# Kernel tuning notes

Measured on AMD Instinct MI355X. Metric: run time of the kernel, lower is better.

The kernel has to match this reference:

```python
import jax, jax.numpy as jnp
import numpy as np

B, T, C = 128, 256, 384
H, HD = 8, 48          # num_heads, head_dim
WINDOW = 64

def setup_inputs() -> dict:
    key = jax.random.key(0)
    ks = jax.random.split(key, 5)
    return {
        "x": jax.random.normal(ks[0], (B, T, C), dtype=jnp.float32),
        "W_qkv": jax.random.normal(ks[1], (C, 3 * C), dtype=jnp.float32) * (1.0 / np.sqrt(C)),
        "b_qkv": jax.random.normal(ks[2], (3 * C,), dtype=jnp.float32) * 0.02,
        "W_proj": jax.random.normal(ks[3], (C, C), dtype=jnp.float32) * (1.0 / np.sqrt(C)),
        "b_proj": jax.random.normal(ks[4], (C,), dtype=jnp.float32) * 0.02,
        "gate": jnp.ones((C,), dtype=jnp.float32),
    }

def reference(x, W_qkv, b_qkv, W_proj, b_proj, gate):
    Bx, Tx, Cx = x.shape
    qkv = x @ W_qkv + b_qkv                                   # [B,T,3C]
    q, k, v = jnp.split(qkv, 3, axis=-1)
    q = q.reshape(Bx, Tx, H, HD).transpose(0, 2, 1, 3)        # [B,H,T,hd]
    k = k.reshape(Bx, Tx, H, HD).transpose(0, 2, 1, 3)
    v = v.reshape(Bx, Tx, H, HD).transpose(0, 2, 1, 3)
    scale = 1.0 / np.sqrt(HD).astype(np.float32)
    att = jnp.einsum("bhqd,bhkd->bhqk", q, k) * scale        # [B,H,T,T]
    idx = jnp.arange(Tx)
    causal = idx[:, None] >= idx[None, :]                     # lower-tri
    local = jnp.abs(idx[None, :] - idx[:, None]) <= WINDOW
    mask = (causal & local)[None, None, :, :]
    att = jnp.where(mask, att, -jnp.inf)
    att = jax.nn.softmax(att, axis=-1)
    out = jnp.einsum("bhqk,bhkd->bhqd", att, v)               # [B,H,T,hd]
    out = out.transpose(0, 2, 1, 3).reshape(Bx, Tx, Cx)       # [B,T,C]
    return (out * gate) @ W_proj + b_proj
```

## Files before the change

### kernel.cpp

```cpp
#include <hip/hip_runtime.h>
#include <hip/hip_bf16.h>

typedef __attribute__((ext_vector_type(8))) short bf16x8;
typedef __attribute__((ext_vector_type(4))) float floatx4;

#define NB 128
#define NT 256
#define NC 384
#define NH 8
#define ND 48

static __device__ __forceinline__ unsigned short f2bf(float f) {
  __hip_bfloat16 h = __float2bfloat16(f);
  return __builtin_bit_cast(unsigned short, h);
}

static __device__ __forceinline__ void gload16(const unsigned short* g, unsigned short* l) {
  __builtin_amdgcn_global_load_lds(
      (const __attribute__((address_space(1))) void*)g,
      (__attribute__((address_space(3))) void*)l, 16, 0, 0);
}

__global__ __launch_bounds__(256) void k_prep(const float* __restrict__ x,
                                              const float* __restrict__ Wq,
                                              const float* __restrict__ Wp,
                                              const float* __restrict__ gate,
                                              unsigned short* __restrict__ xbf,
                                              unsigned short* __restrict__ WqT,
                                              unsigned short* __restrict__ WpT) {
  const int blk = blockIdx.x;
  const int t = threadIdx.x;
  if (blk < 144) {
    __shared__ float T[64][65];
    const float* src;
    unsigned short* dst;
    int N, kt, nt;
    const bool isWp = (blk >= 108);
    if (!isWp) { src = Wq; dst = WqT; N = 1152; kt = blk / 18; nt = blk % 18; }
    else { int b2 = blk - 108; src = Wp; dst = WpT; N = 384; kt = b2 / 6; nt = b2 % 6; }
    const int k0 = kt * 64, n0 = nt * 64;
    const int r = t >> 2, c = (t & 3) * 16;
    const float* s = src + (size_t)(k0 + r) * N + n0 + c;
#pragma unroll
    for (int i = 0; i < 4; ++i) *(float4*)&T[r][c + i * 4] = ((const float4*)s)[i];
    __syncthreads();
    float gv[16];
    if (isWp) {
#pragma unroll
      for (int i = 0; i < 4; ++i) *(float4*)&gv[i * 4] = ((const float4*)(gate + k0 + c))[i];
    } else {
#pragma unroll
      for (int i = 0; i < 16; ++i) gv[i] = 1.f;
    }
    unsigned short o[16];
#pragma unroll
    for (int i = 0; i < 16; ++i) o[i] = f2bf(T[c + i][r] * gv[i]);
    unsigned short* dp = dst + (size_t)(n0 + r) * 384 + k0 + c;
    *(bf16x8*)dp = *(bf16x8*)&o[0];
    *(bf16x8*)(dp + 8) = *(bf16x8*)&o[8];
  } else {
    const int n8 = (NB * NT * NC) / 8;
    int idx = (blk - 144) * 256 + t;
    const int stride = (gridDim.x - 144) * 256;
    for (; idx < n8; idx += stride) {
      const float* s = x + (size_t)idx * 8;
      float v[8];
      *(float4*)&v[0] = ((const float4*)s)[0];
      *(float4*)&v[4] = ((const float4*)s)[1];
      bf16x8 p;
#pragma unroll
      for (int i = 0; i < 8; ++i) p[i] = f2bf(v[i]);
      *(bf16x8*)(xbf + (size_t)idx * 8) = p;
    }
  }
}

#define STAGE_G(Ag, Bg, As, Bs, k0, buf)                                             \
  {                                                                                  \
    const int r0_ = (lane >> 2), sw0_ = 8 * ((lane & 3) ^ ((r0_ >> 1) & 3));         \
    const int r1_ = r0_ + 16,    sw1_ = 8 * ((lane & 3) ^ ((r1_ >> 1) & 3));         \
    gload16(Ag + (size_t)r0_ * 384 + (k0) + sw0_, As + (buf)*4096 + (w * 32) * 32);  \
    gload16(Ag + (size_t)r1_ * 384 + (k0) + sw1_, As + (buf)*4096 + (w * 32 + 16) * 32); \
    gload16(Bg + (size_t)r0_ * 384 + (k0) + sw0_, Bs + (buf)*4096 + (w * 32) * 32);  \
    gload16(Bg + (size_t)r1_ * 384 + (k0) + sw1_, Bs + (buf)*4096 + (w * 32 + 16) * 32); \
  }

#define GEMM_PIPE(Ag, Bg, As, Bs)                                                    \
  STAGE_G(Ag, Bg, As, Bs, 0, 0);                                                     \
  STAGE_G(Ag, Bg, As, Bs, 32, 1);                                                    \
  _Pragma("unroll") for (int t_ = 0; t_ < 12; ++t_) {                                \
    if (t_ < 11) asm volatile("s_waitcnt vmcnt(4)" ::: "memory");                    \
    else         asm volatile("s_waitcnt vmcnt(0)" ::: "memory");                    \
    __builtin_amdgcn_s_barrier();                                                    \
    if (t_ < 10) STAGE_G(Ag, Bg, As, Bs, (t_ + 2) * 32, (t_ + 2) % 3);               \
    const unsigned short* Ac_ = As + (t_ % 3) * 4096;                                \
    const unsigned short* Bc_ = Bs + (t_ % 3) * 4096;                                \
    bf16x8 a_[4], b_[4];                                                             \
    _Pragma("unroll") for (int mt = 0; mt < 4; ++mt) {                               \
      const int R = wm * 64 + mt * 16 + lq;                                          \
      a_[mt] = *(const bf16x8*)&Ac_[R * 32 + 8 * (lg ^ ((R >> 1) & 3))];             \
    }                                                                                \
    _Pragma("unroll") for (int nt = 0; nt < 4; ++nt) {                               \
      const int R = wn * 64 + nt * 16 + lq;                                          \
      b_[nt] = *(const bf16x8*)&Bc_[R * 32 + 8 * (lg ^ ((R >> 1) & 3))];             \
    }                                                                                \
    _Pragma("unroll") for (int mt = 0; mt < 4; ++mt)                                 \
      _Pragma("unroll") for (int nt = 0; nt < 4; ++nt)                               \
        acc[mt][nt] = __builtin_amdgcn_mfma_f32_16x16x32_bf16(a_[mt], b_[nt], acc[mt][nt], 0, 0, 0); \
  }

__global__ __launch_bounds__(256) void k_qkv(const unsigned short* __restrict__ xb,
                                             const unsigned short* __restrict__ WqT,
                                             const float* __restrict__ bq,
                                             unsigned short* __restrict__ qkv) {
  __shared__ __align__(16) unsigned short As[3 * 128 * 32];
  __shared__ __align__(16) unsigned short Bs[3 * 128 * 32];
  const int t = threadIdx.x, lane = t & 63, w = t >> 6;
  const int wm = w >> 1, wn = w & 1;
  const int lq = lane & 15, lg = lane >> 4;
  const int swz = (blockIdx.x & 7) * 288 + (blockIdx.x >> 3);
  const int m0 = (swz / 9) * 128, n0 = (swz % 9) * 128;
  const unsigned short* Ag = xb + (size_t)(m0 + w * 32) * 384;
  const unsigned short* Bg = WqT + (size_t)(n0 + w * 32) * 384;
  floatx4 acc[4][4] = {};

  GEMM_PIPE(Ag, Bg, As, Bs);

#pragma unroll
  for (int nt = 0; nt < 4; ++nt) {
    const int col = n0 + wn * 64 + nt * 16 + lq;
    const float bias = bq[col];
#pragma unroll
    for (int mt = 0; mt < 4; ++mt)
#pragma unroll
      for (int j = 0; j < 4; ++j) {
        const int row = m0 + wm * 64 + mt * 16 + lg * 4 + j;
        qkv[(size_t)row * 1152 + col] = f2bf(acc[mt][nt][j] + bias);
      }
  }
}

__global__ __launch_bounds__(256) void k_proj(const unsigned short* __restrict__ A,
                                              const unsigned short* __restrict__ WpT,
                                              const float* __restrict__ bp,
                                              float* __restrict__ out) {
  __shared__ __align__(16) unsigned short As[3 * 128 * 32];
  __shared__ __align__(16) unsigned short Bs[3 * 128 * 32];
  const int t = threadIdx.x, lane = t & 63, w = t >> 6;
  const int wm = w >> 1, wn = w & 1;
  const int lq = lane & 15, lg = lane >> 4;
  const int swz = (blockIdx.x & 7) * 96 + (blockIdx.x >> 3);
  const int m0 = (swz / 3) * 128, n0 = (swz % 3) * 128;
  const unsigned short* Ag = A + (size_t)(m0 + w * 32) * 384;
  const unsigned short* Bg = WpT + (size_t)(n0 + w * 32) * 384;
  floatx4 acc[4][4] = {};

  GEMM_PIPE(Ag, Bg, As, Bs);

#pragma unroll
  for (int nt = 0; nt < 4; ++nt) {
    const int col = n0 + wn * 64 + nt * 16 + lq;
    const float bias = bp[col];
#pragma unroll
    for (int mt = 0; mt < 4; ++mt)
#pragma unroll
      for (int j = 0; j < 4; ++j) {
        const int row = m0 + wm * 64 + mt * 16 + lg * 4 + j;
        out[(size_t)row * 384 + col] = acc[mt][nt][j] + bias;
      }
  }
}

__global__ __launch_bounds__(256) void k_attn(const unsigned short* __restrict__ qkv,
                                              unsigned short* __restrict__ attg) {
  __shared__ __align__(16) unsigned short Ks[128 * 72];
  __shared__ __align__(16) unsigned short Vt[48 * 152];
  __shared__ __align__(16) unsigned short Ps[4 * 16 * 104];
  const int t = threadIdx.x;
  const int blk = blockIdx.x;
  const int tile = blk & 3;
  const int bh = blk >> 2;
  const int b = bh >> 3, h = bh & 7;
  const int base = tile * 64;
  const unsigned short* qbase = qkv + (size_t)(b * NT) * 1152 + h * 48;
  const unsigned short* kbase = qbase + 384;
  const unsigned short* vbase = qbase + 768;

  if (t < 48) {
    bf16x8 z = {};
    *(bf16x8*)&Vt[t * 152 + 128] = z;
    *(bf16x8*)&Vt[t * 152 + 136] = z;
  }
  if (t < 128) {
    const int r = t, ka = base - 64 + r;
    unsigned short* dst = &Ks[r * 72];
    if (ka >= 0) {
      const unsigned short* src = kbase + (size_t)ka * 1152;
#pragma unroll
      for (int i = 0; i < 6; ++i) *(bf16x8*)(dst + i * 8) = *(const bf16x8*)(src + i * 8);
      bf16x8 z = {};
      *(bf16x8*)(dst + 48) = z;
      *(bf16x8*)(dst + 56) = z;
    } else {
      bf16x8 z = {};
#pragma unroll
      for (int i = 0; i < 8; ++i) *(bf16x8*)(dst + i * 8) = z;
    }
  } else {
    const int r = t - 128, ka = base - 64 + r;
    if (ka >= 0) {
      const unsigned short* src = vbase + (size_t)ka * 1152;
      bf16x8 vv[6];
#pragma unroll
      for (int i = 0; i < 6; ++i) vv[i] = *(const bf16x8*)(src + i * 8);
#pragma unroll
      for (int i = 0; i < 6; ++i)
#pragma unroll
        for (int j = 0; j < 8; ++j)
          Vt[(i * 8 + j) * 152 + r] = (unsigned short)vv[i][j];
    } else {
#pragma unroll
      for (int d = 0; d < 48; ++d) Vt[d * 152 + r] = 0;
    }
  }
  __syncthreads();

  const int lane = t & 63, w = t >> 6;
  const int lq = lane & 15, lg = lane >> 4;
  const int qs = base + w * 16;

  const unsigned short* qrow = qbase + (size_t)(qs + lq) * 1152;
  bf16x8 aq0 = *(const bf16x8*)(qrow + lg * 8);
  bf16x8 aq1 = {};
  if (lg < 2) aq1 = *(const bf16x8*)(qrow + 32 + lg * 8);

  floatx4 s[5];
#pragma unroll
  for (int kt = 0; kt < 5; ++kt) {
    const unsigned short* kr = &Ks[(w * 16 + kt * 16 + lq) * 72];
    bf16x8 kb0 = *(const bf16x8*)(kr + lg * 8);
    bf16x8 kb1 = *(const bf16x8*)(kr + 32 + lg * 8);
    floatx4 z = {};
    z = __builtin_amdgcn_mfma_f32_16x16x32_bf16(aq0, kb0, z, 0, 0, 0);
    z = __builtin_amdgcn_mfma_f32_16x16x32_bf16(aq1, kb1, z, 0, 0, 0);
    s[kt] = z;
  }

  const float scale = 0.14433756729740643f;
  floatx4 pj[5];
#pragma unroll
  for (int j = 0; j < 4; ++j) {
    const int qa = qs + lg * 4 + j;
    float mx = -1e30f;
    float sv[5];
    bool ok[5];
#pragma unroll
    for (int kt = 0; kt < 5; ++kt) {
      const int ka = base - 64 + w * 16 + kt * 16 + lq;
      sv[kt] = s[kt][j] * scale;
      ok[kt] = (ka >= 0) && (ka <= qa) && (qa - ka <= 64);
      if (ok[kt]) mx = fmaxf(mx, sv[kt]);
    }
#pragma unroll
    for (int dd = 1; dd < 16; dd <<= 1) mx = fmaxf(mx, __shfl_xor(mx, dd));
    float sum = 0.f;
#pragma unroll
    for (int kt = 0; kt < 5; ++kt) {
      float p = ok[kt] ? __expf(sv[kt] - mx) : 0.f;
      pj[kt][j] = p;
      sum += p;
    }
#pragma unroll
    for (int dd = 1; dd < 16; dd <<= 1) sum += __shfl_xor(sum, dd);
    const float inv = 1.f / sum;
#pragma unroll
    for (int kt = 0; kt < 5; ++kt) pj[kt][j] *= inv;
  }

  unsigned short* pw = &Ps[w * 16 * 104];
#pragma unroll
  for (int kt = 0; kt < 5; ++kt)
#pragma unroll
    for (int j = 0; j < 4; ++j)
      pw[(lg * 4 + j) * 104 + kt * 16 + lq] = f2bf(pj[kt][j]);
#pragma unroll
  for (int j = 0; j < 4; ++j) pw[lq * 104 + 80 + lg * 4 + j] = 0;

  floatx4 o[3] = {};
#pragma unroll
  for (int c = 0; c < 3; ++c) {
    bf16x8 ap = *(const bf16x8*)&pw[lq * 104 + c * 32 + lg * 8];
#pragma unroll
    for (int nt = 0; nt < 3; ++nt) {
      bf16x8 av = *(const bf16x8*)&Vt[(nt * 16 + lq) * 152 + w * 16 + c * 32 + lg * 8];
      o[nt] = __builtin_amdgcn_mfma_f32_16x16x32_bf16(ap, av, o[nt], 0, 0, 0);
    }
  }
#pragma unroll
  for (int nt = 0; nt < 3; ++nt) {
    const int d = nt * 16 + lq;
    const int c = h * ND + d;
#pragma unroll
    for (int j = 0; j < 4; ++j) {
      const int tt = qs + lg * 4 + j;
      attg[((size_t)b * NT + tt) * NC + c] = f2bf(o[nt][j]);
    }
  }
}

extern "C" void kernel_launch(void* const* d_in, const int* in_sizes, int n_in,
                              void* d_out, int out_size, void* d_ws, size_t ws_size,
                              hipStream_t stream) {
  const float* x    = (const float*)d_in[0];
  const float* Wq   = (const float*)d_in[1];
  const float* bq   = (const float*)d_in[2];
  const float* Wp   = (const float*)d_in[3];
  const float* bp   = (const float*)d_in[4];
  const float* gate = (const float*)d_in[5];

  const size_t nx = (size_t)NB * NT * NC;
  unsigned short* attg = (unsigned short*)d_ws;
  unsigned short* xbf  = attg + nx;
  unsigned short* qkvp = xbf + nx;
  unsigned short* WqT  = qkvp + (size_t)NB * NT * 1152;
  unsigned short* WpT  = WqT + (size_t)384 * 1152;
  float* out = (float*)d_out;

  k_prep<<<dim3(1680), 256, 0, stream>>>(x, Wq, Wp, gate, xbf, WqT, WpT);
  k_qkv<<<dim3(2304), 256, 0, stream>>>(xbf, WqT, bq, qkvp);
  k_attn<<<dim3(4096), 256, 0, stream>>>(qkvp, attg);
  k_proj<<<dim3(768), 256, 0, stream>>>(attg, WpT, bp, out);
}
```

Measured before the change: 121.8 us.

## Restructure GEMMs with resident B tile and write QKV in head-major planes

Both GEMMs now load a full 48x384 weight slice into LDS once per block and give each wave its own 64-row A stream. This removes the block-wide barriers from the k-loop. The QKV GEMM stages its output through LDS and writes it as contiguous [comp][b,h][T][48] planes, so the attention kernel reads K, V and Q rows with unit stride instead of a 1152-element stride. The cost is smaller N tiles (48 wide) with less reuse of A per block, more blocks, and higher LDS use per block, which may lower occupancy.

```diff
diff --git a/kernel.cpp b/kernel.cpp
--- a/kernel.cpp
+++ b/kernel.cpp
@@ -9,6 +9,7 @@
 #define NC 384
 #define NH 8
 #define ND 48
+#define CPLANE (128 * 8 * 256 * 48)
 
 static __device__ __forceinline__ unsigned short f2bf(float f) {
   __hip_bfloat16 h = __float2bfloat16(f);
@@ -75,37 +76,48 @@
   }
 }
 
-#define STAGE_G(Ag, Bg, As, Bs, k0, buf)                                             \
-  {                                                                                  \
-    const int r0_ = (lane >> 2), sw0_ = 8 * ((lane & 3) ^ ((r0_ >> 1) & 3));         \
-    const int r1_ = r0_ + 16,    sw1_ = 8 * ((lane & 3) ^ ((r1_ >> 1) & 3));         \
-    gload16(Ag + (size_t)r0_ * 384 + (k0) + sw0_, As + (buf)*4096 + (w * 32) * 32);  \
-    gload16(Ag + (size_t)r1_ * 384 + (k0) + sw1_, As + (buf)*4096 + (w * 32 + 16) * 32); \
-    gload16(Bg + (size_t)r0_ * 384 + (k0) + sw0_, Bs + (buf)*4096 + (w * 32) * 32);  \
-    gload16(Bg + (size_t)r1_ * 384 + (k0) + sw1_, Bs + (buf)*4096 + (w * 32 + 16) * 32); \
-  }
-
-#define GEMM_PIPE(Ag, Bg, As, Bs)                                                    \
-  STAGE_G(Ag, Bg, As, Bs, 0, 0);                                                     \
-  STAGE_G(Ag, Bg, As, Bs, 32, 1);                                                    \
-  _Pragma("unroll") for (int t_ = 0; t_ < 12; ++t_) {                                \
-    if (t_ < 11) asm volatile("s_waitcnt vmcnt(4)" ::: "memory");                    \
-    else         asm volatile("s_waitcnt vmcnt(0)" ::: "memory");                    \
-    __builtin_amdgcn_s_barrier();                                                    \
-    if (t_ < 10) STAGE_G(Ag, Bg, As, Bs, (t_ + 2) * 32, (t_ + 2) % 3);               \
-    const unsigned short* Ac_ = As + (t_ % 3) * 4096;                                \
-    const unsigned short* Bc_ = Bs + (t_ % 3) * 4096;                                \
-    bf16x8 a_[4], b_[4];                                                             \
-    _Pragma("unroll") for (int mt = 0; mt < 4; ++mt) {                               \
-      const int R = wm * 64 + mt * 16 + lq;                                          \
-      a_[mt] = *(const bf16x8*)&Ac_[R * 32 + 8 * (lg ^ ((R >> 1) & 3))];             \
-    }                                                                                \
-    _Pragma("unroll") for (int nt = 0; nt < 4; ++nt) {                               \
-      const int R = wn * 64 + nt * 16 + lq;                                          \
-      b_[nt] = *(const bf16x8*)&Bc_[R * 32 + 8 * (lg ^ ((R >> 1) & 3))];             \
-    }                                                                                \
-    _Pragma("unroll") for (int mt = 0; mt < 4; ++mt)                                 \
-      _Pragma("unroll") for (int nt = 0; nt < 4; ++nt)                               \
+#define STAGE_A(k0, buf)                                                              \
+  {                                                                                   \
+    _Pragma("unroll") for (int g = 0; g < 4; ++g) {                                   \
+      const int r_ = (lane >> 2) + 16 * g;                                            \
+      gload16(Ag + (size_t)r_ * 384 + (k0) + 8 * ((lane & 3) ^ ((r_ >> 1) & 3)),      \
+              Asl + (buf)*2048 + g * 512);                                            \
+    }                                                                                 \
+  }
+
+#define STAGE_B(WT)                                                                   \
+  {                                                                                   \
+    _Pragma("unroll") for (int cc = 0; cc < 9; ++cc) {                                \
+      const int idx_ = cc * 256 + t;                                                  \
+      const int r_ = idx_ / 48, kc_ = idx_ - r_ * 48;                                 \
+      bf16x8 v_ = *(const bf16x8*)((WT) + (size_t)(n0 + r_) * 384 + kc_ * 8);         \
+      *(bf16x8*)&Bs[r_ * 384 + 8 * (kc_ ^ (r_ & 7))] = v_;                            \
+    }                                                                                 \
+  }
+
+#define GEMM_NOBAR()                                                                  \
+  STAGE_A(0, 0);                                                                      \
+  STAGE_A(32, 1);                                                                     \
+  __syncthreads();                                  \
+  _Pragma("unroll") for (int t_ = 0; t_ < 12; ++t_) {                                 \
+    if (t_ < 11) asm volatile("s_waitcnt vmcnt(4)" ::: "memory");                     \
+    else         asm volatile("s_waitcnt vmcnt(0)" ::: "memory");                     \
+    __builtin_amdgcn_sched_barrier(0);                                                \
+    const unsigned short* Ac_ = Asl + (t_ & 1) * 2048;                                \
+    bf16x8 a_[4], b_[3];                                                              \
+    _Pragma("unroll") for (int mt = 0; mt < 4; ++mt) {                                \
+      const int R = mt * 16 + lq;                                                     \
+      a_[mt] = *(const bf16x8*)&Ac_[R * 32 + 8 * (lg ^ ((R >> 1) & 3))];              \
+    }                                                                                 \
+    _Pragma("unroll") for (int nt = 0; nt < 3; ++nt) {                                \
+      const int R = nt * 16 + lq;                                                     \
+      b_[nt] = *(const bf16x8*)&Bs[R * 384 + 8 * ((t_ * 4 + lg) ^ (R & 7))];          \
+    }                                                                                 \
+    asm volatile("s_waitcnt lgkmcnt(0)" ::: "memory");                                \
+    __builtin_amdgcn_sched_barrier(0);                                                \
+    if (t_ < 10) STAGE_A((t_ + 2) * 32, t_ & 1);                                      \
+    _Pragma("unroll") for (int mt = 0; mt < 4; ++mt)                                  \
+      _Pragma("unroll") for (int nt = 0; nt < 3; ++nt)                                \
         acc[mt][nt] = __builtin_amdgcn_mfma_f32_16x16x32_bf16(a_[mt], b_[nt], acc[mt][nt], 0, 0, 0); \
   }
 
@@ -113,30 +125,39 @@
                                              const unsigned short* __restrict__ WqT,
                                              const float* __restrict__ bq,
                                              unsigned short* __restrict__ qkv) {
-  __shared__ __align__(16) unsigned short As[3 * 128 * 32];
-  __shared__ __align__(16) unsigned short Bs[3 * 128 * 32];
+  __shared__ __align__(16) unsigned short Bs[48 * 384];
+  __shared__ __align__(16) unsigned short As[4 * 4096];
   const int t = threadIdx.x, lane = t & 63, w = t >> 6;
-  const int wm = w >> 1, wn = w & 1;
   const int lq = lane & 15, lg = lane >> 4;
-  const int swz = (blockIdx.x & 7) * 288 + (blockIdx.x >> 3);
-  const int m0 = (swz / 9) * 128, n0 = (swz % 9) * 128;
-  const unsigned short* Ag = xb + (size_t)(m0 + w * 32) * 384;
-  const unsigned short* Bg = WqT + (size_t)(n0 + w * 32) * 384;
-  floatx4 acc[4][4] = {};
-
-  GEMM_PIPE(Ag, Bg, As, Bs);
-
-#pragma unroll
-  for (int nt = 0; nt < 4; ++nt) {
-    const int col = n0 + wn * 64 + nt * 16 + lq;
-    const float bias = bq[col];
+  const int swz = (blockIdx.x & 7) * 384 + (blockIdx.x >> 3);
+  const int mblk = swz / 24, nblk = swz % 24;
+  const int m0 = mblk * 256, n0 = nblk * 48;
+  const unsigned short* Ag = xb + (size_t)(m0 + w * 64) * 384;
+  unsigned short* Asl = As + w * 4096;
+
+  STAGE_B(WqT);
+  floatx4 acc[4][3] = {};
+  GEMM_NOBAR();
+
+  const int comp = nblk >> 3, h = nblk & 7;
+#pragma unroll
+  for (int nt = 0; nt < 3; ++nt) {
+    const float bias = bq[n0 + nt * 16 + lq];
 #pragma unroll
     for (int mt = 0; mt < 4; ++mt)
 #pragma unroll
       for (int j = 0; j < 4; ++j) {
-        const int row = m0 + wm * 64 + mt * 16 + lg * 4 + j;
-        qkv[(size_t)row * 1152 + col] = f2bf(acc[mt][nt][j] + bias);
+        const int r = mt * 16 + lg * 4 + j;
+        Asl[r * 48 + nt * 16 + lq] = f2bf(acc[mt][nt][j] + bias);
       }
+  }
+  asm volatile("s_waitcnt lgkmcnt(0)" ::: "memory");
+  __builtin_amdgcn_sched_barrier(0);
+  const size_t base = (size_t)comp * CPLANE + ((size_t)(mblk * 8 + h) * 256 + w * 64) * 48;
+#pragma unroll
+  for (int i = 0; i < 6; ++i) {
+    bf16x8 v = *(const bf16x8*)&Asl[i * 512 + lane * 8];
+    *(bf16x8*)(qkv + base + i * 512 + lane * 8) = v;
   }
 }
 
@@ -144,28 +165,29 @@
                                               const unsigned short* __restrict__ WpT,
                                               const float* __restrict__ bp,
                                               float* __restrict__ out) {
-  __shared__ __align__(16) unsigned short As[3 * 128 * 32];
-  __shared__ __align__(16) unsigned short Bs[3 * 128 * 32];
+  __shared__ __align__(16) unsigned short Bs[48 * 384];
+  __shared__ __align__(16) unsigned short As[4 * 4096];
   const int t = threadIdx.x, lane = t & 63, w = t >> 6;
-  const int wm = w >> 1, wn = w & 1;
   const int lq = lane & 15, lg = lane >> 4;
-  const int swz = (blockIdx.x & 7) * 96 + (blockIdx.x >> 3);
-  const int m0 = (swz / 3) * 128, n0 = (swz % 3) * 128;
-  const unsigned short* Ag = A + (size_t)(m0 + w * 32) * 384;
-  const unsigned short* Bg = WpT + (size_t)(n0 + w * 32) * 384;
-  floatx4 acc[4][4] = {};
-
-  GEMM_PIPE(Ag, Bg, As, Bs);
-
-#pragma unroll
-  for (int nt = 0; nt < 4; ++nt) {
-    const int col = n0 + wn * 64 + nt * 16 + lq;
+  const int swz = (blockIdx.x & 7) * 128 + (blockIdx.x >> 3);
+  const int mblk = swz / 8, nblk = swz % 8;
+  const int m0 = mblk * 256, n0 = nblk * 48;
+  const unsigned short* Ag = A + (size_t)(m0 + w * 64) * 384;
+  unsigned short* Asl = As + w * 4096;
+
+  STAGE_B(WpT);
+  floatx4 acc[4][3] = {};
+  GEMM_NOBAR();
+
+#pragma unroll
+  for (int nt = 0; nt < 3; ++nt) {
+    const int col = n0 + nt * 16 + lq;
     const float bias = bp[col];
 #pragma unroll
     for (int mt = 0; mt < 4; ++mt)
 #pragma unroll
       for (int j = 0; j < 4; ++j) {
-        const int row = m0 + wm * 64 + mt * 16 + lg * 4 + j;
+        const int row = m0 + w * 64 + mt * 16 + lg * 4 + j;
         out[(size_t)row * 384 + col] = acc[mt][nt][j] + bias;
       }
   }
@@ -182,9 +204,10 @@
   const int bh = blk >> 2;
   const int b = bh >> 3, h = bh & 7;
   const int base = tile * 64;
-  const unsigned short* qbase = qkv + (size_t)(b * NT) * 1152 + h * 48;
-  const unsigned short* kbase = qbase + 384;
-  const unsigned short* vbase = qbase + 768;
+  const size_t kvoff = (size_t)bh * NT * ND;
+  const unsigned short* qptr = qkv + kvoff;
+  const unsigned short* kptr = qkv + (size_t)CPLANE + kvoff;
+  const unsigned short* vptr = qkv + (size_t)2 * CPLANE + kvoff;
 
   if (t < 48) {
     bf16x8 z = {};
@@ -195,7 +218,7 @@
     const int r = t, ka = base - 64 + r;
     unsigned short* dst = &Ks[r * 72];
     if (ka >= 0) {
-      const unsigned short* src = kbase + (size_t)ka * 1152;
+      const unsigned short* src = kptr + (size_t)ka * ND;
 #pragma unroll
       for (int i = 0; i < 6; ++i) *(bf16x8*)(dst + i * 8) = *(const bf16x8*)(src + i * 8);
       bf16x8 z = {};
@@ -209,7 +232,7 @@
   } else {
     const int r = t - 128, ka = base - 64 + r;
     if (ka >= 0) {
-      const unsigned short* src = vbase + (size_t)ka * 1152;
+      const unsigned short* src = vptr + (size_t)ka * ND;
       bf16x8 vv[6];
 #pragma unroll
       for (int i = 0; i < 6; ++i) vv[i] = *(const bf16x8*)(src + i * 8);
@@ -229,7 +252,7 @@
   const int lq = lane & 15, lg = lane >> 4;
   const int qs = base + w * 16;
 
-  const unsigned short* qrow = qbase + (size_t)(qs + lq) * 1152;
+  const unsigned short* qrow = qptr + (size_t)(qs + lq) * ND;
   bf16x8 aq0 = *(const bf16x8*)(qrow + lg * 8);
   bf16x8 aq1 = {};
   if (lg < 2) aq1 = *(const bf16x8*)(qrow + 32 + lg * 8);
@@ -322,12 +345,12 @@
   unsigned short* attg = (unsigned short*)d_ws;
   unsigned short* xbf  = attg + nx;
   unsigned short* qkvp = xbf + nx;
-  unsigned short* WqT  = qkvp + (size_t)NB * NT * 1152;
+  unsigned short* WqT  = qkvp + (size_t)3 * CPLANE;
   unsigned short* WpT  = WqT + (size_t)384 * 1152;
   float* out = (float*)d_out;
 
   k_prep<<<dim3(1680), 256, 0, stream>>>(x, Wq, Wp, gate, xbf, WqT, WpT);
-  k_qkv<<<dim3(2304), 256, 0, stream>>>(xbf, WqT, bq, qkvp);
+  k_qkv<<<dim3(3072), 256, 0, stream>>>(xbf, WqT, bq, qkvp);
   k_attn<<<dim3(4096), 256, 0, stream>>>(qkvp, attg);
-  k_proj<<<dim3(768), 256, 0, stream>>>(attg, WpT, bp, out);
-}
+  k_proj<<<dim3(1024), 256, 0, stream>>>(attg, WpT, bp, out);
+}
```

Measured after the change: 122.6 us. No clear change (+0.7%).

## Write QKV in head-major planes via LDS-staged epilogue, two M-tiles per block

Applied to the files above, without the earlier changes.

The QKV GEMM now writes its output as separate Q, K and V planes in [B,H,T,48] layout. The epilogue is staged through LDS so each lane stores 16-byte vectors instead of scattered 2-byte writes. Each block computes two 128-row M tiles in sequence, halving the grid and reusing the same B-tile stream with prefetch carried across the boundary. The attention kernel reads contiguous 48-element rows, and the GEMM pipeline is manually unrolled. This adds LDS round trips and waits in the epilogue.

```diff
diff --git a/kernel.cpp b/kernel.cpp
--- a/kernel.cpp
+++ b/kernel.cpp
@@ -9,6 +9,7 @@
 #define NC 384
 #define NH 8
 #define ND 48
+#define CPLANE (128 * 8 * 256 * 48)
 
 static __device__ __forceinline__ unsigned short f2bf(float f) {
   __hip_bfloat16 h = __float2bfloat16(f);
@@ -75,26 +76,23 @@
   }
 }
 
-#define STAGE_G(Ag, Bg, As, Bs, k0, buf)                                             \
+#define STAGE_G(Ag, Bg, k0, buf)                                                     \
   {                                                                                  \
     const int r0_ = (lane >> 2), sw0_ = 8 * ((lane & 3) ^ ((r0_ >> 1) & 3));         \
     const int r1_ = r0_ + 16,    sw1_ = 8 * ((lane & 3) ^ ((r1_ >> 1) & 3));         \
-    gload16(Ag + (size_t)r0_ * 384 + (k0) + sw0_, As + (buf)*4096 + (w * 32) * 32);  \
-    gload16(Ag + (size_t)r1_ * 384 + (k0) + sw1_, As + (buf)*4096 + (w * 32 + 16) * 32); \
-    gload16(Bg + (size_t)r0_ * 384 + (k0) + sw0_, Bs + (buf)*4096 + (w * 32) * 32);  \
-    gload16(Bg + (size_t)r1_ * 384 + (k0) + sw1_, Bs + (buf)*4096 + (w * 32 + 16) * 32); \
-  }
-
-#define GEMM_PIPE(Ag, Bg, As, Bs)                                                    \
-  STAGE_G(Ag, Bg, As, Bs, 0, 0);                                                     \
-  STAGE_G(Ag, Bg, As, Bs, 32, 1);                                                    \
-  _Pragma("unroll") for (int t_ = 0; t_ < 12; ++t_) {                                \
-    if (t_ < 11) asm volatile("s_waitcnt vmcnt(4)" ::: "memory");                    \
-    else         asm volatile("s_waitcnt vmcnt(0)" ::: "memory");                    \
-    __builtin_amdgcn_s_barrier();                                                    \
-    if (t_ < 10) STAGE_G(Ag, Bg, As, Bs, (t_ + 2) * 32, (t_ + 2) % 3);               \
-    const unsigned short* Ac_ = As + (t_ % 3) * 4096;                                \
-    const unsigned short* Bc_ = Bs + (t_ % 3) * 4096;                                \
+    gload16((Ag) + (size_t)r0_ * 384 + (k0) + sw0_, As + (buf)*4096 + (w * 32) * 32);  \
+    gload16((Ag) + (size_t)r1_ * 384 + (k0) + sw1_, As + (buf)*4096 + (w * 32 + 16) * 32); \
+    gload16((Bg) + (size_t)r0_ * 384 + (k0) + sw0_, Bs + (buf)*4096 + (w * 32) * 32);  \
+    gload16((Bg) + (size_t)r1_ * 384 + (k0) + sw1_, Bs + (buf)*4096 + (w * 32 + 16) * 32); \
+  }
+
+#define QITER(vmstr, gmod3, STG)                                                     \
+  asm volatile("s_waitcnt vmcnt(" vmstr ")" ::: "memory");                           \
+  __builtin_amdgcn_s_barrier();                                                      \
+  STG;                                                                               \
+  {                                                                                  \
+    const unsigned short* Ac_ = As + (gmod3) * 4096;                                 \
+    const unsigned short* Bc_ = Bs + (gmod3) * 4096;                                 \
     bf16x8 a_[4], b_[4];                                                             \
     _Pragma("unroll") for (int mt = 0; mt < 4; ++mt) {                               \
       const int R = wm * 64 + mt * 16 + lq;                                          \
@@ -109,43 +107,94 @@
         acc[mt][nt] = __builtin_amdgcn_mfma_f32_16x16x32_bf16(a_[mt], b_[nt], acc[mt][nt], 0, 0, 0); \
   }
 
+#define QEPI(m0)                                                                     \
+  __builtin_amdgcn_s_barrier();                                                      \
+  {                                                                                  \
+    unsigned short* Ew = ((w < 2) ? As : Bs) + 2 * 4096 + (w & 1) * 2048;            \
+    _Pragma("unroll") for (int p = 0; p < 4; ++p) {                                  \
+      _Pragma("unroll") for (int nt = 0; nt < 4; ++nt)                               \
+        _Pragma("unroll") for (int j = 0; j < 4; ++j)                                \
+          Ew[(lg * 4 + j) * 72 + nt * 16 + lq] = f2bf(acc[p][nt][j] + bias[nt]);     \
+      asm volatile("s_waitcnt lgkmcnt(0)" ::: "memory");                             \
+      __builtin_amdgcn_sched_barrier(0);                                             \
+      _Pragma("unroll") for (int cc = 0; cc < 2; ++cc) {                             \
+        const int c = cc * 64 + lane;                                                \
+        const int r16 = c >> 3, k8 = c & 7;                                          \
+        bf16x8 v = *(const bf16x8*)&Ew[r16 * 72 + k8 * 8];                           \
+        const int lc = n0 - comp * 384 + wn * 64 + k8 * 8;                           \
+        const int hh = lc / 48, d0 = lc - hh * 48;                                   \
+        const int R = (m0) + wm * 64 + p * 16 + r16;                                 \
+        *(bf16x8*)(qkv + (size_t)comp * CPLANE +                                     \
+                   (((size_t)((R >> 8) * 8 + hh) * 256 + (R & 255)) * 48 + d0)) = v; \
+      }                                                                              \
+      asm volatile("s_waitcnt lgkmcnt(0)" ::: "memory");                             \
+      __builtin_amdgcn_sched_barrier(0);                                             \
+    }                                                                                \
+  }
+
 __global__ __launch_bounds__(256) void k_qkv(const unsigned short* __restrict__ xb,
                                              const unsigned short* __restrict__ WqT,
                                              const float* __restrict__ bq,
                                              unsigned short* __restrict__ qkv) {
-  __shared__ __align__(16) unsigned short As[3 * 128 * 32];
-  __shared__ __align__(16) unsigned short Bs[3 * 128 * 32];
+  __shared__ __align__(16) unsigned short As[3 * 4096];
+  __shared__ __align__(16) unsigned short Bs[3 * 4096];
   const int t = threadIdx.x, lane = t & 63, w = t >> 6;
   const int wm = w >> 1, wn = w & 1;
   const int lq = lane & 15, lg = lane >> 4;
-  const int swz = (blockIdx.x & 7) * 288 + (blockIdx.x >> 3);
-  const int m0 = (swz / 9) * 128, n0 = (swz % 9) * 128;
-  const unsigned short* Ag = xb + (size_t)(m0 + w * 32) * 384;
+  const int swz = (blockIdx.x & 7) * 144 + (blockIdx.x >> 3);
+  const int mp = swz / 9, nblk = swz % 9;
+  const int n0 = nblk * 128;
+  const int comp = n0 / 384;
+  const unsigned short* Ag0 = xb + (size_t)(mp * 256 + w * 32) * 384;
+  const unsigned short* Ag1 = Ag0 + (size_t)128 * 384;
   const unsigned short* Bg = WqT + (size_t)(n0 + w * 32) * 384;
+
+  float bias[4];
+#pragma unroll
+  for (int nt = 0; nt < 4; ++nt) bias[nt] = bq[n0 + wn * 64 + nt * 16 + lq];
+
   floatx4 acc[4][4] = {};
-
-  GEMM_PIPE(Ag, Bg, As, Bs);
-
-#pragma unroll
-  for (int nt = 0; nt < 4; ++nt) {
-    const int col = n0 + wn * 64 + nt * 16 + lq;
-    const float bias = bq[col];
-#pragma unroll
-    for (int mt = 0; mt < 4; ++mt)
-#pragma unroll
-      for (int j = 0; j < 4; ++j) {
-        const int row = m0 + wm * 64 + mt * 16 + lg * 4 + j;
-        qkv[(size_t)row * 1152 + col] = f2bf(acc[mt][nt][j] + bias);
-      }
-  }
+  STAGE_G(Ag0, Bg, 0, 0);
+  STAGE_G(Ag0, Bg, 32, 1);
+  QITER("4", 0, STAGE_G(Ag0, Bg, 64, 2));
+  QITER("4", 1, STAGE_G(Ag0, Bg, 96, 0));
+  QITER("4", 2, STAGE_G(Ag0, Bg, 128, 1));
+  QITER("4", 0, STAGE_G(Ag0, Bg, 160, 2));
+  QITER("4", 1, STAGE_G(Ag0, Bg, 192, 0));
+  QITER("4", 2, STAGE_G(Ag0, Bg, 224, 1));
+  QITER("4", 0, STAGE_G(Ag0, Bg, 256, 2));
+  QITER("4", 1, STAGE_G(Ag0, Bg, 288, 0));
+  QITER("4", 2, STAGE_G(Ag0, Bg, 320, 1));
+  QITER("4", 0, STAGE_G(Ag0, Bg, 352, 2));
+  QITER("4", 1, STAGE_G(Ag1, Bg, 0, 0));
+  QITER("4", 2, {});
+  QEPI(mp * 256);
+  STAGE_G(Ag1, Bg, 32, 1);
+#pragma unroll
+  for (int mt = 0; mt < 4; ++mt)
+#pragma unroll
+    for (int nt = 0; nt < 4; ++nt) acc[mt][nt] = (floatx4){0.f, 0.f, 0.f, 0.f};
+  QITER("12", 0, STAGE_G(Ag1, Bg, 64, 2));
+  QITER("4", 1, STAGE_G(Ag1, Bg, 96, 0));
+  QITER("4", 2, STAGE_G(Ag1, Bg, 128, 1));
+  QITER("4", 0, STAGE_G(Ag1, Bg, 160, 2));
+  QITER("4", 1, STAGE_G(Ag1, Bg, 192, 0));
+  QITER("4", 2, STAGE_G(Ag1, Bg, 224, 1));
+  QITER("4", 0, STAGE_G(Ag1, Bg, 256, 2));
+  QITER("4", 1, STAGE_G(Ag1, Bg, 288, 0));
+  QITER("4", 2, STAGE_G(Ag1, Bg, 320, 1));
+  QITER("4", 0, STAGE_G(Ag1, Bg, 352, 2));
+  QITER("4", 1, {});
+  QITER("0", 2, {});
+  QEPI(mp * 256 + 128);
 }
 
 __global__ __launch_bounds__(256) void k_proj(const unsigned short* __restrict__ A,
                                               const unsigned short* __restrict__ WpT,
                                               const float* __restrict__ bp,
                                               float* __restrict__ out) {
-  __shared__ __align__(16) unsigned short As[3 * 128 * 32];
-  __shared__ __align__(16) unsigned short Bs[3 * 128 * 32];
+  __shared__ __align__(16) unsigned short As[3 * 4096];
+  __shared__ __align__(16) unsigned short Bs[3 * 4096];
   const int t = threadIdx.x, lane = t & 63, w = t >> 6;
   const int wm = w >> 1, wn = w & 1;
   const int lq = lane & 15, lg = lane >> 4;
@@ -155,7 +204,20 @@
   const unsigned short* Bg = WpT + (size_t)(n0 + w * 32) * 384;
   floatx4 acc[4][4] = {};
 
-  GEMM_PIPE(Ag, Bg, As, Bs);
+  STAGE_G(Ag, Bg, 0, 0);
+  STAGE_G(Ag, Bg, 32, 1);
+  QITER("4", 0, STAGE_G(Ag, Bg, 64, 2));
+  QITER("4", 1, STAGE_G(Ag, Bg, 96, 0));
+  QITER("4", 2, STAGE_G(Ag, Bg, 128, 1));
+  QITER("4", 0, STAGE_G(Ag, Bg, 160, 2));
+  QITER("4", 1, STAGE_G(Ag, Bg, 192, 0));
+  QITER("4", 2, STAGE_G(Ag, Bg, 224, 1));
+  QITER("4", 0, STAGE_G(Ag, Bg, 256, 2));
+  QITER("4", 1, STAGE_G(Ag, Bg, 288, 0));
+  QITER("4", 2, STAGE_G(Ag, Bg, 320, 1));
+  QITER("4", 0, STAGE_G(Ag, Bg, 352, 2));
+  QITER("4", 1, {});
+  QITER("0", 2, {});
 
 #pragma unroll
   for (int nt = 0; nt < 4; ++nt) {
@@ -182,9 +244,10 @@
   const int bh = blk >> 2;
   const int b = bh >> 3, h = bh & 7;
   const int base = tile * 64;
-  const unsigned short* qbase = qkv + (size_t)(b * NT) * 1152 + h * 48;
-  const unsigned short* kbase = qbase + 384;
-  const unsigned short* vbase = qbase + 768;
+  const size_t kvoff = (size_t)bh * NT * ND;
+  const unsigned short* qptr = qkv + kvoff;
+  const unsigned short* kptr = qkv + (size_t)CPLANE + kvoff;
+  const unsigned short* vptr = qkv + (size_t)2 * CPLANE + kvoff;
 
   if (t < 48) {
     bf16x8 z = {};
@@ -195,7 +258,7 @@
     const int r = t, ka = base - 64 + r;
     unsigned short* dst = &Ks[r * 72];
     if (ka >= 0) {
-      const unsigned short* src = kbase + (size_t)ka * 1152;
+      const unsigned short* src = kptr + (size_t)ka * ND;
 #pragma unroll
       for (int i = 0; i < 6; ++i) *(bf16x8*)(dst + i * 8) = *(const bf16x8*)(src + i * 8);
       bf16x8 z = {};
@@ -209,7 +272,7 @@
   } else {
     const int r = t - 128, ka = base - 64 + r;
     if (ka >= 0) {
-      const unsigned short* src = vbase + (size_t)ka * 1152;
+      const unsigned short* src = vptr + (size_t)ka * ND;
       bf16x8 vv[6];
 #pragma unroll
       for (int i = 0; i < 6; ++i) vv[i] = *(const bf16x8*)(src + i * 8);
@@ -229,7 +292,7 @@
   const int lq = lane & 15, lg = lane >> 4;
   const int qs = base + w * 16;
 
-  const unsigned short* qrow = qbase + (size_t)(qs + lq) * 1152;
+  const unsigned short* qrow = qptr + (size_t)(qs + lq) * ND;
   bf16x8 aq0 = *(const bf16x8*)(qrow + lg * 8);
   bf16x8 aq1 = {};
   if (lg < 2) aq1 = *(const bf16x8*)(qrow + 32 + lg * 8);
@@ -322,12 +385,12 @@
   unsigned short* attg = (unsigned short*)d_ws;
   unsigned short* xbf  = attg + nx;
   unsigned short* qkvp = xbf + nx;
-  unsigned short* WqT  = qkvp + (size_t)NB * NT * 1152;
+  unsigned short* WqT  = qkvp + (size_t)3 * CPLANE;
   unsigned short* WpT  = WqT + (size_t)384 * 1152;
   float* out = (float*)d_out;
 
   k_prep<<<dim3(1680), 256, 0, stream>>>(x, Wq, Wp, gate, xbf, WqT, WpT);
-  k_qkv<<<dim3(2304), 256, 0, stream>>>(xbf, WqT, bq, qkvp);
+  k_qkv<<<dim3(1152), 256, 0, stream>>>(xbf, WqT, bq, qkvp);
   k_attn<<<dim3(4096), 256, 0, stream>>>(qkvp, attg);
   k_proj<<<dim3(768), 256, 0, stream>>>(attg, WpT, bp, out);
 }
```

New measurement: 121.7 us. About the same (-0.1%).

## Write QKV in head-major planes via LDS-staged vectorized epilogue

Applied to the files above, without the earlier changes.

The QKV GEMM epilogue now stages each 16-row slice of bf16 results in free LDS pipeline buffers. It then writes them as 16-byte vectors into separate Q/K/V planes laid out [B,H,T,48], replacing the old scattered 2-byte stores into a [B*T,1152] row. The attention kernel reads Q, K and V rows contiguously (48 elements per row) instead of striding by 1152. The aim is better store coalescing in the GEMM and denser reads in attention, at the cost of an extra LDS round trip and barriers in the epilogue.

```diff
diff --git a/kernel.cpp b/kernel.cpp
--- a/kernel.cpp
+++ b/kernel.cpp
@@ -9,6 +9,7 @@
 #define NC 384
 #define NH 8
 #define ND 48
+#define CPLANE (128 * 8 * 256 * 48)
 
 static __device__ __forceinline__ unsigned short f2bf(float f) {
   __hip_bfloat16 h = __float2bfloat16(f);
@@ -75,24 +76,24 @@
   }
 }
 
-#define STAGE_G(Ag, Bg, As, Bs, k0, buf)                                             \
+#define STAGE_G(Ag, Bg, k0, buf)                                                     \
   {                                                                                  \
     const int r0_ = (lane >> 2), sw0_ = 8 * ((lane & 3) ^ ((r0_ >> 1) & 3));         \
     const int r1_ = r0_ + 16,    sw1_ = 8 * ((lane & 3) ^ ((r1_ >> 1) & 3));         \
-    gload16(Ag + (size_t)r0_ * 384 + (k0) + sw0_, As + (buf)*4096 + (w * 32) * 32);  \
-    gload16(Ag + (size_t)r1_ * 384 + (k0) + sw1_, As + (buf)*4096 + (w * 32 + 16) * 32); \
-    gload16(Bg + (size_t)r0_ * 384 + (k0) + sw0_, Bs + (buf)*4096 + (w * 32) * 32);  \
-    gload16(Bg + (size_t)r1_ * 384 + (k0) + sw1_, Bs + (buf)*4096 + (w * 32 + 16) * 32); \
-  }
-
-#define GEMM_PIPE(Ag, Bg, As, Bs)                                                    \
-  STAGE_G(Ag, Bg, As, Bs, 0, 0);                                                     \
-  STAGE_G(Ag, Bg, As, Bs, 32, 1);                                                    \
+    gload16((Ag) + (size_t)r0_ * 384 + (k0) + sw0_, As + (buf)*4096 + (w * 32) * 32);  \
+    gload16((Ag) + (size_t)r1_ * 384 + (k0) + sw1_, As + (buf)*4096 + (w * 32 + 16) * 32); \
+    gload16((Bg) + (size_t)r0_ * 384 + (k0) + sw0_, Bs + (buf)*4096 + (w * 32) * 32);  \
+    gload16((Bg) + (size_t)r1_ * 384 + (k0) + sw1_, Bs + (buf)*4096 + (w * 32 + 16) * 32); \
+  }
+
+#define GEMM_PIPE(Ag, Bg)                                                            \
+  STAGE_G(Ag, Bg, 0, 0);                                                             \
+  STAGE_G(Ag, Bg, 32, 1);                                                            \
   _Pragma("unroll") for (int t_ = 0; t_ < 12; ++t_) {                                \
     if (t_ < 11) asm volatile("s_waitcnt vmcnt(4)" ::: "memory");                    \
     else         asm volatile("s_waitcnt vmcnt(0)" ::: "memory");                    \
     __builtin_amdgcn_s_barrier();                                                    \
-    if (t_ < 10) STAGE_G(Ag, Bg, As, Bs, (t_ + 2) * 32, (t_ + 2) % 3);               \
+    if (t_ < 10) STAGE_G(Ag, Bg, (t_ + 2) * 32, (t_ + 2) % 3);                       \
     const unsigned short* Ac_ = As + (t_ % 3) * 4096;                                \
     const unsigned short* Bc_ = Bs + (t_ % 3) * 4096;                                \
     bf16x8 a_[4], b_[4];                                                             \
@@ -113,30 +114,46 @@
                                              const unsigned short* __restrict__ WqT,
                                              const float* __restrict__ bq,
                                              unsigned short* __restrict__ qkv) {
-  __shared__ __align__(16) unsigned short As[3 * 128 * 32];
-  __shared__ __align__(16) unsigned short Bs[3 * 128 * 32];
+  __shared__ __align__(16) unsigned short As[3 * 4096];
+  __shared__ __align__(16) unsigned short Bs[3 * 4096];
   const int t = threadIdx.x, lane = t & 63, w = t >> 6;
   const int wm = w >> 1, wn = w & 1;
   const int lq = lane & 15, lg = lane >> 4;
   const int swz = (blockIdx.x & 7) * 288 + (blockIdx.x >> 3);
   const int m0 = (swz / 9) * 128, n0 = (swz % 9) * 128;
+  const int comp = n0 / 384;
   const unsigned short* Ag = xb + (size_t)(m0 + w * 32) * 384;
   const unsigned short* Bg = WqT + (size_t)(n0 + w * 32) * 384;
   floatx4 acc[4][4] = {};
 
-  GEMM_PIPE(Ag, Bg, As, Bs);
-
-#pragma unroll
-  for (int nt = 0; nt < 4; ++nt) {
-    const int col = n0 + wn * 64 + nt * 16 + lq;
-    const float bias = bq[col];
-#pragma unroll
-    for (int mt = 0; mt < 4; ++mt)
-#pragma unroll
-      for (int j = 0; j < 4; ++j) {
-        const int row = m0 + wm * 64 + mt * 16 + lg * 4 + j;
-        qkv[(size_t)row * 1152 + col] = f2bf(acc[mt][nt][j] + bias);
-      }
+  GEMM_PIPE(Ag, Bg);
+
+  __builtin_amdgcn_s_barrier();
+  unsigned short* Ew = ((w < 2) ? As : Bs) + 2 * 4096 + (w & 1) * 2048;
+#pragma unroll
+  for (int p = 0; p < 4; ++p) {
+#pragma unroll
+    for (int nt = 0; nt < 4; ++nt) {
+      const float bias = bq[n0 + wn * 64 + nt * 16 + lq];
+#pragma unroll
+      for (int j = 0; j < 4; ++j)
+        Ew[(lg * 4 + j) * 72 + nt * 16 + lq] = f2bf(acc[p][nt][j] + bias);
+    }
+    asm volatile("s_waitcnt lgkmcnt(0)" ::: "memory");
+    __builtin_amdgcn_sched_barrier(0);
+#pragma unroll
+    for (int cc = 0; cc < 2; ++cc) {
+      const int c = cc * 64 + lane;
+      const int r16 = c >> 3, k8 = c & 7;
+      bf16x8 v = *(const bf16x8*)&Ew[r16 * 72 + k8 * 8];
+      const int lc = n0 - comp * 384 + wn * 64 + k8 * 8;
+      const int hh = lc / 48, d0 = lc - hh * 48;
+      const int R = m0 + wm * 64 + p * 16 + r16;
+      *(bf16x8*)(qkv + (size_t)comp * CPLANE +
+                 (((size_t)((R >> 8) * 8 + hh) * 256 + (R & 255)) * 48 + d0)) = v;
+    }
+    asm volatile("s_waitcnt lgkmcnt(0)" ::: "memory");
+    __builtin_amdgcn_sched_barrier(0);
   }
 }
 
@@ -144,8 +161,8 @@
                                               const unsigned short* __restrict__ WpT,
                                               const float* __restrict__ bp,
                                               float* __restrict__ out) {
-  __shared__ __align__(16) unsigned short As[3 * 128 * 32];
-  __shared__ __align__(16) unsigned short Bs[3 * 128 * 32];
+  __shared__ __align__(16) unsigned short As[3 * 4096];
+  __shared__ __align__(16) unsigned short Bs[3 * 4096];
   const int t = threadIdx.x, lane = t & 63, w = t >> 6;
   const int wm = w >> 1, wn = w & 1;
   const int lq = lane & 15, lg = lane >> 4;
@@ -155,7 +172,7 @@
   const unsigned short* Bg = WpT + (size_t)(n0 + w * 32) * 384;
   floatx4 acc[4][4] = {};
 
-  GEMM_PIPE(Ag, Bg, As, Bs);
+  GEMM_PIPE(Ag, Bg);
 
 #pragma unroll
   for (int nt = 0; nt < 4; ++nt) {
@@ -182,9 +199,10 @@
   const int bh = blk >> 2;
   const int b = bh >> 3, h = bh & 7;
   const int base = tile * 64;
-  const unsigned short* qbase = qkv + (size_t)(b * NT) * 1152 + h * 48;
-  const unsigned short* kbase = qbase + 384;
-  const unsigned short* vbase = qbase + 768;
+  const size_t kvoff = (size_t)bh * NT * ND;
+  const unsigned short* qptr = qkv + kvoff;
+  const unsigned short* kptr = qkv + (size_t)CPLANE + kvoff;
+  const unsigned short* vptr = qkv + (size_t)2 * CPLANE + kvoff;
 
   if (t < 48) {
     bf16x8 z = {};
@@ -195,7 +213,7 @@
     const int r = t, ka = base - 64 + r;
     unsigned short* dst = &Ks[r * 72];
     if (ka >= 0) {
-      const unsigned short* src = kbase + (size_t)ka * 1152;
+      const unsigned short* src = kptr + (size_t)ka * ND;
 #pragma unroll
       for (int i = 0; i < 6; ++i) *(bf16x8*)(dst + i * 8) = *(const bf16x8*)(src + i * 8);
       bf16x8 z = {};
@@ -209,7 +227,7 @@
   } else {
     const int r = t - 128, ka = base - 64 + r;
     if (ka >= 0) {
-      const unsigned short* src = vbase + (size_t)ka * 1152;
+      const unsigned short* src = vptr + (size_t)ka * ND;
       bf16x8 vv[6];
 #pragma unroll
       for (int i = 0; i < 6; ++i) vv[i] = *(const bf16x8*)(src + i * 8);
@@ -229,7 +247,7 @@
   const int lq = lane & 15, lg = lane >> 4;
   const int qs = base + w * 16;
 
-  const unsigned short* qrow = qbase + (size_t)(qs + lq) * 1152;
+  const unsigned short* qrow = qptr + (size_t)(qs + lq) * ND;
   bf16x8 aq0 = *(const bf16x8*)(qrow + lg * 8);
   bf16x8 aq1 = {};
   if (lg < 2) aq1 = *(const bf16x8*)(qrow + 32 + lg * 8);
@@ -322,7 +340,7 @@
   unsigned short* attg = (unsigned short*)d_ws;
   unsigned short* xbf  = attg + nx;
   unsigned short* qkvp = xbf + nx;
-  unsigned short* WqT  = qkvp + (size_t)NB * NT * 1152;
+  unsigned short* WqT  = qkvp + (size_t)3 * CPLANE;
   unsigned short* WpT  = WqT + (size_t)384 * 1152;
   float* out = (float*)d_out;
 
```

Result: faster. 113.3 us (-7.0%).
